# Performance work log

Measured on AMD Instinct MI355X. Metric: run time of the kernel, lower is better.

## Reference

```python
import jax, jax.numpy as jnp
import numpy as np

D_MODEL = 2048
NUM_HEADS = 16
NUM_GROUPS = 4
HEAD_DIM = D_MODEL // NUM_HEADS  # 128; note d_model//num_groups == num_groups*head_dim


def setup_inputs() -> dict:
    key = jax.random.key(0)
    ks = jax.random.split(key, 11)
    B, S, D = 4, 1024, D_MODEL
    dk = D // NUM_GROUPS  # 512
    s = 0.02
    return {
        "query": jax.random.normal(ks[0], (B, S, D), jnp.float32),
        "key": jax.random.normal(ks[1], (B, S, D), jnp.float32),
        "value": jax.random.normal(ks[2], (B, S, D), jnp.float32),
        "Wq": jax.random.normal(ks[3], (D, D), jnp.float32) * s,
        "bq": jnp.zeros((D,), jnp.float32),
        "Wk": jax.random.normal(ks[4], (D, dk), jnp.float32) * s,
        "bk": jnp.zeros((dk,), jnp.float32),
        "Wv": jax.random.normal(ks[5], (D, dk), jnp.float32) * s,
        "bv": jnp.zeros((dk,), jnp.float32),
        "Wo": jax.random.normal(ks[6], (D, D), jnp.float32) * s,
        "bo": jnp.zeros((D,), jnp.float32),
    }


def reference(query, key, value, Wq, bq, Wk, bk, Wv, bv, Wo, bo):
    B, S, D = query.shape
    rep = NUM_HEADS // NUM_GROUPS
    # projections
    q = query @ Wq + bq                      # [B,S,D]
    k = key @ Wk + bk                        # [B,S,D//G]
    v = value @ Wv + bv                      # [B,S,D//G]
    # split heads: q -> [B,H,S,hd]; k,v -> [B,G,S,hd] (valid since D//G == G*hd)
    q = q.reshape(B, S, NUM_HEADS, HEAD_DIM).transpose(0, 2, 1, 3)
    k = k.reshape(B, S, NUM_GROUPS, HEAD_DIM).transpose(0, 2, 1, 3)
    v = v.reshape(B, S, NUM_GROUPS, HEAD_DIM).transpose(0, 2, 1, 3)
    # repeat_interleave KV groups to match heads: [B,H,S,hd]
    k = jnp.repeat(k, rep, axis=1)
    v = jnp.repeat(v, rep, axis=1)
    scale = 1.0 / jnp.sqrt(jnp.float32(HEAD_DIM))
    scores = jnp.einsum("bhqd,bhkd->bhqk", q, k) * scale  # [B,H,S,S]
    attn_weights = jax.nn.softmax(scores, axis=-1)
    attn_output = jnp.einsum("bhqk,bhkd->bhqd", attn_weights, v)
    attn_output = attn_output.transpose(0, 2, 1, 3).reshape(B, S, D)
    output = attn_output @ Wo + bo
    return output, attn_weights
```

## Files before the change

### kernel.cpp

```cpp
#include <hip/hip_runtime.h>
#include <hip/hip_bf16.h>

typedef unsigned short u16;
typedef __attribute__((ext_vector_type(8))) short short8;
typedef __attribute__((ext_vector_type(4))) float f32x4;

__device__ __forceinline__ u16 f2bf(float f) {
  __hip_bfloat16 h = __float2bfloat16(f);
  return *reinterpret_cast<u16*>(&h);
}

struct TP4 {
  const float *s0, *s1, *s2, *s3;
  u16 *d0, *d1, *d2, *d3;
};
__global__ __launch_bounds__(256)
void transpose4_kernel(TP4 tp) {
  const int z = blockIdx.z;
  const float* sf; u16* dst; int C;
  if      (z == 0) { sf = tp.s0; dst = tp.d0; C = 2048; }
  else if (z == 1) { sf = tp.s1; dst = tp.d1; C = 512;  }
  else if (z == 2) { sf = tp.s2; dst = tp.d2; C = 512;  }
  else             { sf = tp.s3; dst = tp.d3; C = 2048; }
  const int c0 = blockIdx.x * 32, r0 = blockIdx.y * 32;
  if (c0 >= C) return;
  const int R = 2048;
  __shared__ u16 tile[32][33];
  const int tx = threadIdx.x, ty = threadIdx.y;
#pragma unroll
  for (int i = 0; i < 4; ++i) {
    int r = r0 + ty + i * 8;
    tile[ty + i * 8][tx] = f2bf(sf[(long)r * C + c0 + tx]);
  }
  __syncthreads();
#pragma unroll
  for (int i = 0; i < 4; ++i) {
    int rr = ty + i * 8;
    dst[(long)(c0 + rr) * R + r0 + tx] = tile[tx][rr];
  }
}

#define BM 128
#define BN 128
#define BK 64

struct GemmP {
  const void* A;
  const u16* B;
  const float* bias;
  void* C;
  int N, K, lda, ldb, ldc, mode;
  float scale;
};
struct Gemm3 {
  GemmP q[3];
  int nb0, nb1;
  int nwg;
};

template<bool AF32>
__global__ __launch_bounds__(256, 2)
void gemm3_kernel(Gemm3 g) {
  __shared__ __align__(16) u16 lds[2][2][BM * BK];
  const int t = threadIdx.x;
  const int w = t >> 6, l = t & 63;

  const int cpx = g.nwg >> 3;
  const int swz = (blockIdx.x & 7) * cpx + (blockIdx.x >> 3);
  int pi, local;
  if (swz < g.nb0)            { pi = 0; local = swz; }
  else if (swz < g.nb0 + g.nb1) { pi = 1; local = swz - g.nb0; }
  else                        { pi = 2; local = swz - g.nb0 - g.nb1; }
  const GemmP p = g.q[pi];

  const int nTn = p.N / BN;
  const int tm = (local / nTn) * BM;
  const int tn = (local % nTn) * BN;

  const u16*   Ab = (const u16*)p.A + (long)tm * p.lda;
  const float* Af = (const float*)p.A + (long)tm * p.lda;
  const u16*   Bt = p.B + (long)tn * p.ldb;

  const int wr = w >> 1, wc = w & 1;
  f32x4 acc[4][4] = {};
  float aR[32];

  auto stageB = [&](int kt, int buf) {
#pragma unroll
    for (int i = 0; i < 4; ++i) {
      int c = i * 256 + t;
      int row = c >> 3;
      int slot = (c & 7) ^ (row & 7);
      const u16* gp = Bt + kt * BK + (long)row * p.ldb + slot * 8;
      u16* lp = &lds[buf][1][(i * 256 + w * 64) * 8];
      __builtin_amdgcn_global_load_lds(
          (const __attribute__((address_space(1))) unsigned int*)gp,
          (__attribute__((address_space(3))) unsigned int*)lp, 16, 0, 0);
    }
  };
  auto stageA_bf16 = [&](int kt, int buf) {
#pragma unroll
    for (int i = 0; i < 4; ++i) {
      int c = i * 256 + t;
      int row = c >> 3;
      int slot = (c & 7) ^ (row & 7);
      const u16* gp = Ab + kt * BK + (long)row * p.lda + slot * 8;
      u16* lp = &lds[buf][0][(i * 256 + w * 64) * 8];
      __builtin_amdgcn_global_load_lds(
          (const __attribute__((address_space(1))) unsigned int*)gp,
          (__attribute__((address_space(3))) unsigned int*)lp, 16, 0, 0);
    }
  };
  auto loadA_f32 = [&](int kt) {
    const float* g0 = Af + kt * BK;
#pragma unroll
    for (int i = 0; i < 4; ++i) {
      int c = i * 256 + t;
      int row = c >> 3, slot = c & 7;
      const float4* gp = (const float4*)(g0 + (long)row * p.lda + slot * 8);
      float4 v0 = gp[0], v1 = gp[1];
      aR[i * 8 + 0] = v0.x; aR[i * 8 + 1] = v0.y; aR[i * 8 + 2] = v0.z; aR[i * 8 + 3] = v0.w;
      aR[i * 8 + 4] = v1.x; aR[i * 8 + 5] = v1.y; aR[i * 8 + 6] = v1.z; aR[i * 8 + 7] = v1.w;
    }
  };
  auto writeA = [&](int buf) {
#pragma unroll
    for (int i = 0; i < 4; ++i) {
      int c = i * 256 + t;
      int row = c >> 3, slot = c & 7;
      short8 o;
#pragma unroll
      for (int j = 0; j < 8; ++j) o[j] = (short)f2bf(aR[i * 8 + j]);
      *(short8*)&lds[buf][0][row * 64 + ((slot ^ (row & 7)) * 8)] = o;
    }
  };
  auto compute = [&](int buf) {
    const u16* At  = lds[buf][0];
    const u16* Btl = lds[buf][1];
#pragma unroll
    for (int ks = 0; ks < 2; ++ks) {
      short8 af[4], bfr[4];
#pragma unroll
      for (int mi = 0; mi < 4; ++mi) {
        int row = wr * 64 + mi * 16 + (l & 15);
        int slot = (ks * 4 + (l >> 4)) ^ (row & 7);
        af[mi] = *(const short8*)&At[row * 64 + slot * 8];
      }
#pragma unroll
      for (int ni = 0; ni < 4; ++ni) {
        int row = wc * 64 + ni * 16 + (l & 15);
        int slot = (ks * 4 + (l >> 4)) ^ (row & 7);
        bfr[ni] = *(const short8*)&Btl[row * 64 + slot * 8];
      }
#pragma unroll
      for (int mi = 0; mi < 4; ++mi)
#pragma unroll
        for (int ni = 0; ni < 4; ++ni)
          acc[mi][ni] = __builtin_amdgcn_mfma_f32_16x16x32_bf16(
              af[mi], bfr[ni], acc[mi][ni], 0, 0, 0);
    }
  };

  const int nkt = p.K / BK;
  if (AF32) { loadA_f32(0); stageB(0, 0); writeA(0); }
  else      { stageA_bf16(0, 0); stageB(0, 0); }
  __syncthreads();

  int buf = 0;
  for (int kt = 0; kt < nkt; ++kt) {
    if (kt + 1 < nkt) {
      if (AF32) loadA_f32(kt + 1); else stageA_bf16(kt + 1, buf ^ 1);
      stageB(kt + 1, buf ^ 1);
    }
    compute(buf);
    if (AF32 && kt + 1 < nkt) writeA(buf ^ 1);
    __syncthreads();
    buf ^= 1;
  }

  const int cl = l & 15, rj = (l >> 4) * 4;
#pragma unroll
  for (int mi = 0; mi < 4; ++mi) {
#pragma unroll
    for (int ni = 0; ni < 4; ++ni) {
      int cidx = tn + wc * 64 + ni * 16 + cl;
      float bv = p.bias ? p.bias[cidx] : 0.f;
#pragma unroll
      for (int j = 0; j < 4; ++j) {
        int r = tm + wr * 64 + mi * 16 + rj + j;
        float v = acc[mi][ni][j] * p.scale + bv;
        if (p.mode == 2) {
          ((u16*)p.C)[((long)(r >> 10)) * 524288 + (long)cidx * 1024 + (r & 1023)] = f2bf(v);
        } else {
          long idx = (long)r * p.ldc + cidx;
          if (p.mode == 1) ((u16*)p.C)[idx] = f2bf(v);
          else             ((float*)p.C)[idx] = v;
        }
      }
    }
  }
}

__global__ __launch_bounds__(512, 4)
void fused_attn_kernel(const u16* __restrict__ Qg, const u16* __restrict__ Kg,
                       const u16* __restrict__ Vg, float* __restrict__ attnF,
                       u16* __restrict__ AO) {
  __shared__ __align__(16) u16 kv[2][2][64 * 128];
  __shared__ __align__(16) u16 p4[2][2][32 * 64];
  float* red = (float*)&p4[1][0][0];
  u16* kvf = &kv[0][0][0];

  const int t = threadIdx.x;
  const int w = t >> 6, l = t & 63;
  const int wq = w >> 2, wcol = w & 3;
  const int qb = blockIdx.x, z = blockIdx.y;
  const int b = z >> 4, h = z & 15, g = h >> 2;
  const int q0 = qb * 32;
  const int qi = wq * 16 + (l & 15);

  const u16* Qbase = Qg + ((long)b * 1024 + q0) * 2048 + h * 128;
  const u16* Kbase = Kg + (long)b * 1024 * 512 + g * 128;
  const u16* Vbase = Vg + ((long)b * 512 + g * 128) * 1024;
  float* attnO = attnF + ((long)z * 1024 + q0) * 1024;

  auto glds16 = [](const u16* gp, u16* lp) {
    __builtin_amdgcn_global_load_lds(
        (const __attribute__((address_space(1))) unsigned int*)gp,
        (__attribute__((address_space(3))) unsigned int*)lp, 16, 0, 0);
  };
  auto stageKf = [&](int c, int buf) {
#pragma unroll
    for (int i = 0; i < 2; ++i) {
      int idx = i * 512 + t;
      int row = idx >> 4, blk = idx & 15;
      glds16(Kbase + (long)(c * 64 + row) * 512 + ((blk ^ (row & 7)) * 8),
             &kvf[buf * 8192 + (i * 512 + w * 64) * 8]);
    }
  };
  auto stageVf = [&](int c, int buf) {
#pragma unroll
    for (int i = 0; i < 2; ++i) {
      int idx = i * 512 + t;
      int row = idx >> 3, blk = idx & 7;
      glds16(Vbase + (long)row * 1024 + c * 64 + ((blk ^ (row & 7)) * 8),
             &kvf[buf * 8192 + (i * 512 + w * 64) * 8]);
    }
  };
  auto stageV = [&](int c, int pb, int sub) { stageVf(c, pb * 2 + sub); };

  {
    int row = t >> 4, blk = t & 15;
    glds16(Qbase + (long)row * 2048 + ((blk ^ (row & 7)) * 8), &((u16*)p4)[(w * 64) * 8]);
  }
  stageKf(0, 0);
  stageKf(1, 1);
  stageKf(2, 2);
  asm volatile("s_waitcnt vmcnt(4)" ::: "memory");
  __builtin_amdgcn_sched_barrier(0);
  __builtin_amdgcn_s_barrier();

  short8 qf[4];
  {
    const u16* pq = (const u16*)p4;
#pragma unroll
    for (int ks = 0; ks < 4; ++ks) {
      int slot = (ks * 4 + (l >> 4)) ^ (qi & 7);
      qf[ks] = *(const short8*)&pq[qi * 128 + slot * 8];
    }
  }

  f32x4 acc[16];
#pragma unroll
  for (int c = 0; c < 16; ++c) acc[c] = (f32x4){0.f, 0.f, 0.f, 0.f};

  const int krow = wcol * 16 + (l & 15);
#pragma unroll
  for (int c = 0; c < 16; ++c) {
    const u16* Kl = &kvf[(c & 3) * 8192];
    __builtin_amdgcn_s_setprio(1);
#pragma unroll
    for (int ks = 0; ks < 4; ++ks) {
      int slot = (ks * 4 + (l >> 4)) ^ (krow & 7);
      short8 kf = *(const short8*)&Kl[krow * 128 + slot * 8];
      acc[c] = __builtin_amdgcn_mfma_f32_16x16x32_bf16(kf, qf[ks], acc[c], 0, 0, 0);
    }
    __builtin_amdgcn_s_setprio(0);
    __builtin_amdgcn_s_barrier();
    if (c + 3 < 16)      stageKf(c + 3, (c + 3) & 3);
    else if (c + 3 < 18) stageVf(c + 3 - 16, (c + 3) & 3);
    if (c < 15) {
      asm volatile("s_waitcnt vmcnt(4)" ::: "memory");
      __builtin_amdgcn_sched_barrier(0);
      __builtin_amdgcn_s_barrier();
    }
  }

  const float scale = 0.08838834764831845f;
  float jm[4] = {-1e30f, -1e30f, -1e30f, -1e30f};
#pragma unroll
  for (int c = 0; c < 16; ++c) {
#pragma unroll
    for (int j = 0; j < 4; ++j) jm[j] = fmaxf(jm[j], acc[c][j]);
  }
  float mx = fmaxf(fmaxf(jm[0], jm[1]), fmaxf(jm[2], jm[3]));
  mx = fmaxf(mx, __shfl_xor(mx, 16));
  mx = fmaxf(mx, __shfl_xor(mx, 32));
  if ((l >> 4) == 0) red[wcol * 32 + qi] = mx;
  __syncthreads();
  const float m = fmaxf(fmaxf(red[0 * 32 + qi], red[1 * 32 + qi]),
                        fmaxf(red[2 * 32 + qi], red[3 * 32 + qi]));
  __syncthreads();
  float s4[4] = {0.f, 0.f, 0.f, 0.f};
#pragma unroll
  for (int c = 0; c < 16; ++c) {
#pragma unroll
    for (int j = 0; j < 4; ++j) {
      float e = __expf((acc[c][j] - m) * scale);
      acc[c][j] = e;
      s4[j] += e;
    }
  }
  float ss = (s4[0] + s4[1]) + (s4[2] + s4[3]);
  ss += __shfl_xor(ss, 16);
  ss += __shfl_xor(ss, 32);
  if ((l >> 4) == 0) red[wcol * 32 + qi] = ss;
  __syncthreads();
  const float inv = 1.0f / (red[0 * 32 + qi] + red[1 * 32 + qi] +
                            red[2 * 32 + qi] + red[3 * 32 + qi]);

#pragma unroll
  for (int c = 0; c < 16; ++c) acc[c] = acc[c] * inv;

  const int kloc = wcol * 16 + ((l >> 4) * 4);
  auto pwrite = [&](u16* dst, const f32x4& a) {
    int blk = (kloc >> 3) ^ (qi & 7);
    uint2 val;
    val.x = (unsigned)f2bf(a[0]) | ((unsigned)f2bf(a[1]) << 16);
    val.y = (unsigned)f2bf(a[2]) | ((unsigned)f2bf(a[3]) << 16);
    *(uint2*)&dst[qi * 64 + blk * 8 + (kloc & 7)] = val;
  };

  pwrite(p4[0][0], acc[0]);
  pwrite(p4[0][1], acc[1]);
  __syncthreads();

  f32x4 acc2[2] = {};
  const int prow = wq * 16 + (l & 15);
#pragma unroll
  for (int pp = 0; pp < 8; ++pp) {
    if (pp < 7) {
      pwrite(p4[(pp + 1) & 1][0], acc[2 * pp + 2]);
      pwrite(p4[(pp + 1) & 1][1], acc[2 * pp + 3]);
      stageV(2 * pp + 2, (pp + 1) & 1, 0);
      stageV(2 * pp + 3, (pp + 1) & 1, 1);
    }
    __builtin_amdgcn_s_setprio(1);
#pragma unroll
    for (int sub = 0; sub < 2; ++sub) {
      const u16* Vl = kv[pp & 1][sub];
      const u16* Pl = p4[pp & 1][sub];
#pragma unroll
      for (int ks = 0; ks < 2; ++ks) {
        int ablk = (ks * 4 + (l >> 4)) ^ (prow & 7);
        short8 af = *(const short8*)&Pl[prow * 64 + ablk * 8];
#pragma unroll
        for (int ni = 0; ni < 2; ++ni) {
          int vrow = wcol * 32 + ni * 16 + (l & 15);
          int vslot = (ks * 4 + (l >> 4)) ^ (vrow & 7);
          short8 vf = *(const short8*)&Vl[vrow * 64 + vslot * 8];
          acc2[ni] = __builtin_amdgcn_mfma_f32_16x16x32_bf16(af, vf, acc2[ni], 0, 0, 0);
        }
      }
    }
    __builtin_amdgcn_s_setprio(0);
    __syncthreads();
  }

#pragma unroll
  for (int c = 0; c < 16; ++c)
    *(f32x4*)(attnO + (long)qi * 1024 + c * 64 + wcol * 16 + ((l >> 4) * 4)) = acc[c];

  u16* AObase = AO + ((long)b * 1024 + q0) * 2048 + h * 128;
#pragma unroll
  for (int ni = 0; ni < 2; ++ni)
#pragma unroll
    for (int j = 0; j < 4; ++j) {
      int qq = wq * 16 + (l >> 4) * 4 + j;
      int d = wcol * 32 + ni * 16 + (l & 15);
      AObase[(long)qq * 2048 + d] = f2bf(acc2[ni][j]);
    }
}

extern "C" void kernel_launch(void* const* d_in, const int* in_sizes, int n_in,
                              void* d_out, int out_size, void* d_ws, size_t ws_size,
                              hipStream_t stream) {
  const float* query = (const float*)d_in[0];
  const float* key_  = (const float*)d_in[1];
  const float* value = (const float*)d_in[2];
  const float* Wq = (const float*)d_in[3]; const float* bq = (const float*)d_in[4];
  const float* Wk = (const float*)d_in[5]; const float* bk = (const float*)d_in[6];
  const float* Wv = (const float*)d_in[7]; const float* bv = (const float*)d_in[8];
  const float* Wo = (const float*)d_in[9]; const float* bo = (const float*)d_in[10];

  float* outF  = (float*)d_out;
  float* attnF = outF + 8388608;

  char* wp = (char*)d_ws;
  u16* WqT = (u16*)wp; wp += 2048L * 2048 * 2;
  u16* WkT = (u16*)wp; wp += 512L * 2048 * 2;
  u16* WvT = (u16*)wp; wp += 512L * 2048 * 2;
  u16* WoT = (u16*)wp; wp += 2048L * 2048 * 2;
  u16* Qb  = (u16*)wp; wp += 4096L * 2048 * 2;
  u16* Kb  = (u16*)wp; wp += 4096L * 512 * 2;
  u16* VT  = (u16*)wp; wp += 4L * 512 * 1024 * 2;
  u16* AO  = (u16*)wp; wp += 4096L * 2048 * 2;

  TP4 tp;
  tp.s0 = Wq; tp.s1 = Wk; tp.s2 = Wv; tp.s3 = Wo;
  tp.d0 = WqT; tp.d1 = WkT; tp.d2 = WvT; tp.d3 = WoT;
  transpose4_kernel<<<dim3(64, 64, 4), dim3(32, 8), 0, stream>>>(tp);

  Gemm3 g = {};
  g.q[0].A = query; g.q[0].B = WqT; g.q[0].bias = bq; g.q[0].C = Qb;
  g.q[0].N = 2048; g.q[0].K = 2048; g.q[0].lda = 2048; g.q[0].ldb = 2048;
  g.q[0].ldc = 2048; g.q[0].mode = 1; g.q[0].scale = 1.f;
  g.q[1].A = key_; g.q[1].B = WkT; g.q[1].bias = bk; g.q[1].C = Kb;
  g.q[1].N = 512; g.q[1].K = 2048; g.q[1].lda = 2048; g.q[1].ldb = 2048;
  g.q[1].ldc = 512; g.q[1].mode = 1; g.q[1].scale = 1.f;
  g.q[2].A = value; g.q[2].B = WvT; g.q[2].bias = bv; g.q[2].C = VT;
  g.q[2].N = 512; g.q[2].K = 2048; g.q[2].lda = 2048; g.q[2].ldb = 2048;
  g.q[2].ldc = 1024; g.q[2].mode = 2; g.q[2].scale = 1.f;
  g.nb0 = 512; g.nb1 = 128; g.nwg = 768;
  gemm3_kernel<true><<<dim3(768), 256, 0, stream>>>(g);

  fused_attn_kernel<<<dim3(32, 64), 512, 0, stream>>>(Qb, Kb, VT, attnF, AO);

  Gemm3 go = {};
  go.q[0].A = AO; go.q[0].B = WoT; go.q[0].bias = bo; go.q[0].C = outF;
  go.q[0].N = 2048; go.q[0].K = 2048; go.q[0].lda = 2048; go.q[0].ldb = 2048;
  go.q[0].ldc = 2048; go.q[0].mode = 0; go.q[0].scale = 1.f;
  go.nb0 = 512; go.nb1 = 0; go.nwg = 512;
  gemm3_kernel<false><<<dim3(512), 256, 0, stream>>>(go);
}
```

Before: 295.9 us.

## Write full P tile to LDS once and read V directly from global

The PV phase no longer stages V chunks through LDS with double buffering and per-chunk barriers. Instead, all 16 P chunks are written into the freed K buffer at once, and V fragments are loaded straight from global memory into registers for the MFMA. This removes the staging traffic and 8 block-wide syncs, and the K-loop wait counts are adjusted now that the V prefetch is gone. The cost is that V loads become uncoalesced and latency-exposed global reads sitting directly in the MFMA loop, which relies on L2/L1 hits.

```diff
diff --git a/kernel.cpp b/kernel.cpp
--- a/kernel.cpp
+++ b/kernel.cpp
@@ -205,10 +205,10 @@
 void fused_attn_kernel(const u16* __restrict__ Qg, const u16* __restrict__ Kg,
                        const u16* __restrict__ Vg, float* __restrict__ attnF,
                        u16* __restrict__ AO) {
-  __shared__ __align__(16) u16 kv[2][2][64 * 128];
+  __shared__ __align__(16) u16 kv[4][64 * 128];
   __shared__ __align__(16) u16 p4[2][2][32 * 64];
   float* red = (float*)&p4[1][0][0];
-  u16* kvf = &kv[0][0][0];
+  u16* kvf = &kv[0][0];
 
   const int t = threadIdx.x;
   const int w = t >> 6, l = t & 63;
@@ -237,16 +237,6 @@
              &kvf[buf * 8192 + (i * 512 + w * 64) * 8]);
     }
   };
-  auto stageVf = [&](int c, int buf) {
-#pragma unroll
-    for (int i = 0; i < 2; ++i) {
-      int idx = i * 512 + t;
-      int row = idx >> 3, blk = idx & 7;
-      glds16(Vbase + (long)row * 1024 + c * 64 + ((blk ^ (row & 7)) * 8),
-             &kvf[buf * 8192 + (i * 512 + w * 64) * 8]);
-    }
-  };
-  auto stageV = [&](int c, int pb, int sub) { stageVf(c, pb * 2 + sub); };
 
   {
     int row = t >> 4, blk = t & 15;
@@ -286,10 +276,11 @@
     }
     __builtin_amdgcn_s_setprio(0);
     __builtin_amdgcn_s_barrier();
-    if (c + 3 < 16)      stageKf(c + 3, (c + 3) & 3);
-    else if (c + 3 < 18) stageVf(c + 3 - 16, (c + 3) & 3);
+    if (c + 3 < 16) stageKf(c + 3, (c + 3) & 3);
     if (c < 15) {
-      asm volatile("s_waitcnt vmcnt(4)" ::: "memory");
+      if      (c <= 12) { asm volatile("s_waitcnt vmcnt(4)" ::: "memory"); }
+      else if (c == 13) { asm volatile("s_waitcnt vmcnt(2)" ::: "memory"); }
+      else              { asm volatile("s_waitcnt vmcnt(0)" ::: "memory"); }
       __builtin_amdgcn_sched_barrier(0);
       __builtin_amdgcn_s_barrier();
     }
@@ -332,48 +323,37 @@
   for (int c = 0; c < 16; ++c) acc[c] = acc[c] * inv;
 
   const int kloc = wcol * 16 + ((l >> 4) * 4);
-  auto pwrite = [&](u16* dst, const f32x4& a) {
-    int blk = (kloc >> 3) ^ (qi & 7);
-    uint2 val;
-    val.x = (unsigned)f2bf(a[0]) | ((unsigned)f2bf(a[1]) << 16);
-    val.y = (unsigned)f2bf(a[2]) | ((unsigned)f2bf(a[3]) << 16);
-    *(uint2*)&dst[qi * 64 + blk * 8 + (kloc & 7)] = val;
-  };
-
-  pwrite(p4[0][0], acc[0]);
-  pwrite(p4[0][1], acc[1]);
+  {
+    const int blk = (kloc >> 3) ^ (qi & 7);
+    const int base = qi * 64 + blk * 8 + (kloc & 7);
+#pragma unroll
+    for (int c = 0; c < 16; ++c) {
+      uint2 val;
+      val.x = (unsigned)f2bf(acc[c][0]) | ((unsigned)f2bf(acc[c][1]) << 16);
+      val.y = (unsigned)f2bf(acc[c][2]) | ((unsigned)f2bf(acc[c][3]) << 16);
+      *(uint2*)&kvf[c * 2048 + base] = val;
+    }
+  }
   __syncthreads();
 
   f32x4 acc2[2] = {};
   const int prow = wq * 16 + (l & 15);
-#pragma unroll
-  for (int pp = 0; pp < 8; ++pp) {
-    if (pp < 7) {
-      pwrite(p4[(pp + 1) & 1][0], acc[2 * pp + 2]);
-      pwrite(p4[(pp + 1) & 1][1], acc[2 * pp + 3]);
-      stageV(2 * pp + 2, (pp + 1) & 1, 0);
-      stageV(2 * pp + 3, (pp + 1) & 1, 1);
-    }
+  const int vrow0 = wcol * 32 + (l & 15);
+#pragma unroll 4
+  for (int c2 = 0; c2 < 16; ++c2) {
     __builtin_amdgcn_s_setprio(1);
 #pragma unroll
-    for (int sub = 0; sub < 2; ++sub) {
-      const u16* Vl = kv[pp & 1][sub];
-      const u16* Pl = p4[pp & 1][sub];
-#pragma unroll
-      for (int ks = 0; ks < 2; ++ks) {
-        int ablk = (ks * 4 + (l >> 4)) ^ (prow & 7);
-        short8 af = *(const short8*)&Pl[prow * 64 + ablk * 8];
-#pragma unroll
-        for (int ni = 0; ni < 2; ++ni) {
-          int vrow = wcol * 32 + ni * 16 + (l & 15);
-          int vslot = (ks * 4 + (l >> 4)) ^ (vrow & 7);
-          short8 vf = *(const short8*)&Vl[vrow * 64 + vslot * 8];
-          acc2[ni] = __builtin_amdgcn_mfma_f32_16x16x32_bf16(af, vf, acc2[ni], 0, 0, 0);
-        }
+    for (int ks = 0; ks < 2; ++ks) {
+      int kblk = ks * 4 + (l >> 4);
+      short8 af = *(const short8*)&kvf[c2 * 2048 + prow * 64 + ((kblk ^ (prow & 7)) * 8)];
+#pragma unroll
+      for (int ni = 0; ni < 2; ++ni) {
+        const short8 vf = *(const short8*)&Vbase[(long)(vrow0 + ni * 16) * 1024 +
+                                                c2 * 64 + ks * 32 + ((l >> 4) * 8)];
+        acc2[ni] = __builtin_amdgcn_mfma_f32_16x16x32_bf16(af, vf, acc2[ni], 0, 0, 0);
       }
     }
     __builtin_amdgcn_s_setprio(0);
-    __syncthreads();
   }
 
 #pragma unroll
```

Result: slower. 379.6 us (+28.3%).
